# Optimization experiments

Hardware: AMD Instinct MI355X
Metric: run time of the kernel (lower is better)

Reference implementation:

```python
import jax, jax.numpy as jnp
import numpy as np

COORD_SCALE = 10.0  # spread coords so pairwise dists span the 15/30 A cutoffs


def _cdist(x):
    # pairwise Euclidean distances for x: (b, n, 3) -> (b, n, n)
    sq = jnp.sum(x * x, axis=-1)
    d2 = sq[:, :, None] + sq[:, None, :] - 2.0 * jnp.einsum('bid,bjd->bij', x, x)
    return jnp.sqrt(jnp.clip(d2, 1e-12))  # safe sqrt (diag is 0)


def setup_inputs() -> dict:
    key = jax.random.key(0)
    k1, k2, k3, k4 = jax.random.split(key, 4)
    b, n = 2, 4096
    pred_coords = jax.random.normal(k1, (b, n, 3), dtype=jnp.float32) * COORD_SCALE
    true_coords = pred_coords + jax.random.normal(k2, (b, n, 3), dtype=jnp.float32)
    is_dna = jax.random.bernoulli(k3, 0.25, (b, n))
    is_rna = jax.random.bernoulli(k4, 0.25, (b, n))
    return {"pred_coords": pred_coords, "true_coords": true_coords,
            "is_dna": is_dna, "is_rna": is_rna}


def reference(pred_coords, true_coords, is_dna, is_rna,
              nucleic_acid_cutoff=30.0, other_cutoff=15.0):
    n = pred_coords.shape[1]
    pred_dists = _cdist(pred_coords)              # (b, n, n)
    true_dists = _cdist(true_coords)              # (b, n, n)
    dist_diff = jnp.abs(true_dists - pred_dists)
    eps = (jax.nn.sigmoid(0.5 - dist_diff) + jax.nn.sigmoid(1.0 - dist_diff)
           + jax.nn.sigmoid(2.0 - dist_diff) + jax.nn.sigmoid(4.0 - dist_diff)) / 4.0
    is_nuc = is_dna | is_rna                      # (b, n)
    is_nuc_pair = is_nuc[:, :, None] & is_nuc[:, None, :]
    inclusion = jnp.where(is_nuc_pair,
                          true_dists < nucleic_acid_cutoff,
                          true_dists < other_cutoff)
    mask = inclusion & ~jnp.eye(n, dtype=bool)[None]
    lddt_sum = jnp.sum(eps * mask, axis=(-1, -2))
    lddt_count = jnp.sum(mask, axis=(-1, -2))
    lddt = lddt_sum / jnp.maximum(lddt_count, 1).astype(lddt_sum.dtype)
    return 1.0 - jnp.mean(lddt)
```

## Files before the change

kernel.cpp:

```cpp
#include <hip/hip_runtime.h>
#include <math.h>

#define TPB 128

#define L2E 1.4426950408889634f

#define A1c 1.1280610230094226f
#define A2c 0.3753279228541867f
#define A3c 0.0366994760193147f
#define A4c 0.0005530843701478f
#define B1c 3.3841830690282678f
#define B2c 0.7506558457083734f
#define B3c 0.0366994760193147f
#define EPS_SELF 3.2163290f

typedef float f2 __attribute__((ext_vector_type(2)));

static __device__ __forceinline__ f2 f2fma(f2 a, f2 b, f2 c) {
  return __builtin_elementwise_fma(a, b, c);
}
static __device__ __forceinline__ f2 splat(float x) {
  f2 r; r.x = x; r.y = x; return r;
}

__global__ __launch_bounds__(TPB) void lddt_pairs(
    const float* __restrict__ pred, const float* __restrict__ truec,
    const int* __restrict__ isdna, const int* __restrict__ isrna,
    float2* __restrict__ part, int N, int C)
{
  const int wv   = threadIdx.x >> 6;
  const int lane = threadIdx.x & 63;
  const int t = blockIdx.x * 2 + wv;
  const int b = blockIdx.y;

  const float fC = (float)C;
  int ic = (int)((2.0f*fC + 1.0f -
                  sqrtf((2.0f*fC + 1.0f)*(2.0f*fC + 1.0f) - 8.0f*(float)t)) * 0.5f);
  if (ic > C - 1) ic = C - 1;
  if (ic < 0) ic = 0;
  while (ic > 0 && t < ic*C - ((ic*(ic-1)) >> 1)) --ic;
  while (t >= (ic+1)*C - (((ic+1)*ic) >> 1)) ++ic;
  const int jc = ic + t - (ic*C - ((ic*(ic-1)) >> 1));
  const bool diag = (ic == jc);

  const float C30SQ = (30.0f*L2E)*(30.0f*L2E);
  const float C15SQ = (15.0f*L2E)*(15.0f*L2E);

  __shared__ f2 spx[2][32], spy[2][32], spz[2][32];
  __shared__ f2 stx[2][32], sty[2][32], stz[2][32];
  __shared__ f2 scut[2][32];
  __shared__ float2 blkred[2];

  {
    const int j = jc * 64 + lane;
    const size_t base = (size_t)b * N + j;
    const float* pp = pred  + base * 3;
    const float* tt = truec + base * 3;
    ((float*)spx[wv])[lane] = pp[0]*L2E;
    ((float*)spy[wv])[lane] = pp[1]*L2E;
    ((float*)spz[wv])[lane] = pp[2]*L2E;
    ((float*)stx[wv])[lane] = tt[0]*L2E;
    ((float*)sty[wv])[lane] = tt[1]*L2E;
    ((float*)stz[wv])[lane] = tt[2]*L2E;
    ((float*)scut[wv])[lane] = ((isdna[base] | isrna[base]) != 0) ? C30SQ : C15SQ;
  }

  const int i = ic * 64 + lane;
  const size_t ibase = (size_t)b * N + i;
  const f2 pix2 = splat(pred[ibase*3+0]*L2E);
  const f2 piy2 = splat(pred[ibase*3+1]*L2E);
  const f2 piz2 = splat(pred[ibase*3+2]*L2E);
  const f2 tix2 = splat(truec[ibase*3+0]*L2E);
  const f2 tiy2 = splat(truec[ibase*3+1]*L2E);
  const f2 tiz2 = splat(truec[ibase*3+2]*L2E);
  const bool nuci = ((isdna[ibase] | isrna[ibase]) != 0);

  const f2 vA4 = splat(A4c), vA3 = splat(A3c), vA2 = splat(A2c), vA1 = splat(A1c);
  const f2 vB3 = splat(B3c), vB2 = splat(B2c), vB1 = splat(B1c);
  const f2 v1 = splat(1.0f), v4 = splat(4.0f);
  const f2 vC15 = splat(C15SQ);

  __syncthreads();

  f2  sum2 = splat(0.0f);
  int cnt = 0;

#pragma unroll 8
  for (int k = 0; k < 32; ++k) {
    f2 dx = spx[wv][k] - pix2;
    f2 dy = spy[wv][k] - piy2;
    f2 dz = spz[wv][k] - piz2;
    f2 d2p = f2fma(dx, dx, f2fma(dy, dy, dz * dz));
    f2 ex = stx[wv][k] - tix2;
    f2 ey = sty[wv][k] - tiy2;
    f2 ez = stz[wv][k] - tiz2;
    f2 d2t = f2fma(ex, ex, f2fma(ey, ey, ez * ez));

    f2 dpv, dtv;
    dpv.x = __builtin_amdgcn_sqrtf(d2p.x);
    dpv.y = __builtin_amdgcn_sqrtf(d2p.y);
    dtv.x = __builtin_amdgcn_sqrtf(d2t.x);
    dtv.y = __builtin_amdgcn_sqrtf(d2t.y);
    f2 diff = dtv - dpv;

    f2 e;
    e.x = __builtin_amdgcn_exp2f(fabsf(diff.x));
    e.y = __builtin_amdgcn_exp2f(fabsf(diff.y));

    f2 den = f2fma(f2fma(f2fma(f2fma(vA4, e, vA3), e, vA2), e, vA1), e, v1);
    f2 num = f2fma(f2fma(f2fma(vB3, e, vB2), e, vB1), e, v4);
    f2 r;
    r.x = __builtin_amdgcn_rcpf(den.x);
    r.y = __builtin_amdgcn_rcpf(den.y);
    f2 eps = num * r;

    f2 cutj = scut[wv][k];
    f2 cut = nuci ? cutj : vC15;
    bool i0 = d2t.x < cut.x;
    bool i1 = d2t.y < cut.y;
    cnt += (int)__popcll(__ballot(i0));
    cnt += (int)__popcll(__ballot(i1));
    f2 add;
    add.x = i0 ? eps.x : 0.0f;
    add.y = i1 ? eps.y : 0.0f;
    sum2 += add;
  }

  float sum = sum2.x + sum2.y;
  if (diag) { sum -= EPS_SELF; cnt -= 64; }

  for (int off = 32; off > 0; off >>= 1)
    sum += __shfl_down(sum, off, 64);

  if (lane == 0) {
    const float w = diag ? 1.0f : 2.0f;
    blkred[wv] = make_float2(0.25f * w * sum, w * (float)cnt);
  }
  __syncthreads();
  if (threadIdx.x == 0) {
    const float2 a = blkred[0], c = blkred[1];
    part[(size_t)b * gridDim.x + blockIdx.x] = make_float2(a.x + c.x, a.y + c.y);
  }
}

__global__ __launch_bounds__(1024) void lddt_final(
    const float2* __restrict__ part, float* __restrict__ out, int B, int P)
{
  __shared__ float rs[16], rc[16];
  float acc = 0.0f;
  for (int b = 0; b < B; ++b) {
    float s = 0.0f, c = 0.0f;
    for (int k = threadIdx.x; k < P; k += 1024) {
      const float2 p = part[(size_t)b * P + k];
      s += p.x;
      c += p.y;
    }
    for (int off = 32; off > 0; off >>= 1) {
      s += __shfl_down(s, off, 64);
      c += __shfl_down(c, off, 64);
    }
    const int wave = threadIdx.x >> 6, lane = threadIdx.x & 63;
    if (lane == 0) { rs[wave] = s; rc[wave] = c; }
    __syncthreads();
    if (threadIdx.x == 0) {
      float S = 0.0f, Cc = 0.0f;
      for (int w = 0; w < 16; ++w) { S += rs[w]; Cc += rc[w]; }
      acc += S / fmaxf(Cc, 1.0f);
    }
    __syncthreads();
  }
  if (threadIdx.x == 0) out[0] = 1.0f - acc / (float)B;
}

extern "C" void kernel_launch(void* const* d_in, const int* in_sizes, int n_in,
                              void* d_out, int out_size, void* d_ws, size_t ws_size,
                              hipStream_t stream)
{
  const float* pred  = (const float*)d_in[0];
  const float* truec = (const float*)d_in[1];
  const int*   isdna = (const int*)d_in[2];
  const int*   isrna = (const int*)d_in[3];
  float* out = (float*)d_out;
  float2* part = (float2*)d_ws;

  const int B = 2;
  const int N = in_sizes[2] / B;
  const int C = N / 64;
  const int T = C * (C + 1) / 2;
  const int NB = T / 2;

  dim3 grid(NB, B);
  lddt_pairs<<<grid, TPB, 0, stream>>>(pred, truec, isdna, isrna, part, N, C);
  lddt_final<<<1, 1024, 0, stream>>>(part, out, B, NB);
}
```

Baseline: 76.95 us.

## Split each 64x64 tile across two waves sharing one staged j-tile

```diff
diff --git a/kernel.cpp b/kernel.cpp
--- a/kernel.cpp
+++ b/kernel.cpp
@@ -23,14 +23,14 @@
   f2 r; r.x = x; r.y = x; return r;
 }
 
-__global__ __launch_bounds__(TPB) void lddt_pairs(
+__global__ __launch_bounds__(TPB, 6) void lddt_pairs(
     const float* __restrict__ pred, const float* __restrict__ truec,
     const int* __restrict__ isdna, const int* __restrict__ isrna,
     float2* __restrict__ part, int N, int C)
 {
   const int wv   = threadIdx.x >> 6;
   const int lane = threadIdx.x & 63;
-  const int t = blockIdx.x * 2 + wv;
+  const int t = blockIdx.x;
   const int b = blockIdx.y;
 
   const float fC = (float)C;
@@ -46,54 +46,57 @@
   const float C30SQ = (30.0f*L2E)*(30.0f*L2E);
   const float C15SQ = (15.0f*L2E)*(15.0f*L2E);
 
-  __shared__ f2 spx[2][32], spy[2][32], spz[2][32];
-  __shared__ f2 stx[2][32], sty[2][32], stz[2][32];
-  __shared__ f2 scut[2][32];
+  __shared__ f2 spx[32], spy[32], spz[32];
+  __shared__ f2 stx[32], sty[32], stz[32];
+  __shared__ f2 scut[32];
   __shared__ float2 blkred[2];
 
   {
     const int j = jc * 64 + lane;
-    const size_t base = (size_t)b * N + j;
-    const float* pp = pred  + base * 3;
-    const float* tt = truec + base * 3;
-    ((float*)spx[wv])[lane] = pp[0]*L2E;
-    ((float*)spy[wv])[lane] = pp[1]*L2E;
-    ((float*)spz[wv])[lane] = pp[2]*L2E;
-    ((float*)stx[wv])[lane] = tt[0]*L2E;
-    ((float*)sty[wv])[lane] = tt[1]*L2E;
-    ((float*)stz[wv])[lane] = tt[2]*L2E;
-    ((float*)scut[wv])[lane] = ((isdna[base] | isrna[base]) != 0) ? C30SQ : C15SQ;
+    const size_t jb = (size_t)b * N + j;
+    if (wv == 0) {
+      const float* pp = pred + jb * 3;
+      ((float*)spx)[lane] = pp[0]*L2E;
+      ((float*)spy)[lane] = pp[1]*L2E;
+      ((float*)spz)[lane] = pp[2]*L2E;
+      ((float*)scut)[lane] = ((isdna[jb] | isrna[jb]) != 0) ? C30SQ : C15SQ;
+    } else {
+      const float* tt = truec + jb * 3;
+      ((float*)stx)[lane] = tt[0]*L2E;
+      ((float*)sty)[lane] = tt[1]*L2E;
+      ((float*)stz)[lane] = tt[2]*L2E;
+    }
   }
 
   const int i = ic * 64 + lane;
-  const size_t ibase = (size_t)b * N + i;
-  const f2 pix2 = splat(pred[ibase*3+0]*L2E);
-  const f2 piy2 = splat(pred[ibase*3+1]*L2E);
-  const f2 piz2 = splat(pred[ibase*3+2]*L2E);
-  const f2 tix2 = splat(truec[ibase*3+0]*L2E);
-  const f2 tiy2 = splat(truec[ibase*3+1]*L2E);
-  const f2 tiz2 = splat(truec[ibase*3+2]*L2E);
-  const bool nuci = ((isdna[ibase] | isrna[ibase]) != 0);
+  const size_t ib = (size_t)b * N + i;
+  const f2 pix2 = splat(pred[ib*3+0]*L2E);
+  const f2 piy2 = splat(pred[ib*3+1]*L2E);
+  const f2 piz2 = splat(pred[ib*3+2]*L2E);
+  const f2 tix2 = splat(truec[ib*3+0]*L2E);
+  const f2 tiy2 = splat(truec[ib*3+1]*L2E);
+  const f2 tiz2 = splat(truec[ib*3+2]*L2E);
+  const f2 cuti2 = splat(((isdna[ib] | isrna[ib]) != 0) ? C30SQ : C15SQ);
 
   const f2 vA4 = splat(A4c), vA3 = splat(A3c), vA2 = splat(A2c), vA1 = splat(A1c);
   const f2 vB3 = splat(B3c), vB2 = splat(B2c), vB1 = splat(B1c);
   const f2 v1 = splat(1.0f), v4 = splat(4.0f);
-  const f2 vC15 = splat(C15SQ);
 
   __syncthreads();
 
   f2  sum2 = splat(0.0f);
   int cnt = 0;
 
-#pragma unroll 8
-  for (int k = 0; k < 32; ++k) {
-    f2 dx = spx[wv][k] - pix2;
-    f2 dy = spy[wv][k] - piy2;
-    f2 dz = spz[wv][k] - piz2;
+  const int k0 = wv * 16;
+#pragma unroll 4
+  for (int k = k0; k < k0 + 16; ++k) {
+    f2 dx = spx[k] - pix2;
+    f2 dy = spy[k] - piy2;
+    f2 dz = spz[k] - piz2;
     f2 d2p = f2fma(dx, dx, f2fma(dy, dy, dz * dz));
-    f2 ex = stx[wv][k] - tix2;
-    f2 ey = sty[wv][k] - tiy2;
-    f2 ez = stz[wv][k] - tiz2;
+    f2 ex = stx[k] - tix2;
+    f2 ey = sty[k] - tiy2;
+    f2 ez = stz[k] - tiz2;
     f2 d2t = f2fma(ex, ex, f2fma(ey, ey, ez * ez));
 
     f2 dpv, dtv;
@@ -114,8 +117,7 @@
     r.y = __builtin_amdgcn_rcpf(den.y);
     f2 eps = num * r;
 
-    f2 cutj = scut[wv][k];
-    f2 cut = nuci ? cutj : vC15;
+    f2 cut = __builtin_elementwise_min(cuti2, scut[k]);
     bool i0 = d2t.x < cut.x;
     bool i1 = d2t.y < cut.y;
     cnt += (int)__popcll(__ballot(i0));
@@ -127,7 +129,10 @@
   }
 
   float sum = sum2.x + sum2.y;
-  if (diag) { sum -= EPS_SELF; cnt -= 64; }
+  if (diag) {
+    if ((lane >> 5) == wv) sum -= EPS_SELF;
+    cnt -= 32;
+  }
 
   for (int off = 32; off > 0; off >>= 1)
     sum += __shfl_down(sum, off, 64);
@@ -187,9 +192,8 @@
   const int N = in_sizes[2] / B;
   const int C = N / 64;
   const int T = C * (C + 1) / 2;
-  const int NB = T / 2;
 
-  dim3 grid(NB, B);
+  dim3 grid(T, B);
   lddt_pairs<<<grid, TPB, 0, stream>>>(pred, truec, isdna, isrna, part, N, C);
-  lddt_final<<<1, 1024, 0, stream>>>(part, out, B, NB);
+  lddt_final<<<1, 1024, 0, stream>>>(part, out, B, T);
 }
```

New measurement: 76.18 us (median of 2 runs). Within noise of the previous version (-1.0%).
